# Optimization experiments

Measured on AMD Instinct MI355X. Metric: run time of the kernel, lower is better.

Reference implementation:

```python
import jax, jax.numpy as jnp
import numpy as np

D_MODEL, D_STATE, EXPAND = 1024, 64, 2
D_INNER = EXPAND * D_MODEL
BATCH, SEQ = 4, 2048


def setup_inputs() -> dict:
    key = jax.random.key(0)
    ks = jax.random.split(key, 7)
    s = lambda *d: 1.0 / np.sqrt(d[0])
    x = jax.random.normal(ks[0], (BATCH, SEQ, D_MODEL), dtype=jnp.float32)
    # weights stored as [in, out] so y = x @ W
    W_in = jax.random.normal(ks[1], (D_MODEL, 2 * D_INNER), dtype=jnp.float32) * s(D_MODEL)
    W_xp = jax.random.normal(ks[2], (D_INNER, 2 * D_STATE + 1), dtype=jnp.float32) * s(D_INNER)
    W_B = jax.random.normal(ks[3], (D_STATE, D_INNER), dtype=jnp.float32) * s(D_STATE)
    W_C = jax.random.normal(ks[4], (D_STATE, D_INNER), dtype=jnp.float32) * s(D_STATE)
    W_out = jax.random.normal(ks[5], (D_INNER, D_MODEL), dtype=jnp.float32) * s(D_INNER)
    D = jnp.ones((D_INNER,), dtype=jnp.float32)
    A_log = jnp.asarray(np.log(0.01), dtype=jnp.float32)
    return {"x": x, "W_in": W_in, "W_xp": W_xp, "W_B": W_B,
            "W_C": W_C, "W_out": W_out, "D": D, "A_log": A_log}


def _scan_recurrence(a, b):
    """h_t = a_t * h_{t-1} + b_t via associative scan over seq axis (axis=1).
    a, b: [B, S, D_inner]."""
    def combine(e1, e2):
        a1, b1 = e1
        a2, b2 = e2
        return a1 * a2, a2 * b1 + b2
    _, h = jax.lax.associative_scan(combine, (a, b), axis=1)
    return h


def reference(x, W_in, W_xp, W_B, W_C, W_out, D, A_log):
    xz = x @ W_in                               # [B,S,2*Di]
    xi, z = jnp.split(xz, 2, axis=-1)           # each [B,S,Di]
    proj = xi @ W_xp                            # [B,S,2*Ds+1]
    delta = jax.nn.softplus(proj[..., :1])      # [B,S,1]
    B_raw = proj[..., 1:1 + D_STATE]
    C_raw = proj[..., 1 + D_STATE:]
    B = B_raw @ W_B                             # [B,S,Di]
    C = C_raw @ W_C                             # [B,S,Di]
    A = -jnp.exp(A_log)                         # scalar
    A_bar = jnp.exp(delta * A)                  # [B,S,1]
    a = jnp.broadcast_to(A_bar, B.shape)        # [B,S,Di]
    h = _scan_recurrence(a, B * xi)             # [B,S,Di]
    y = C * h + D * xi                          # [B,S,Di]
    y = y * jax.nn.silu(z)
    return y @ W_out                            # [B,S,Dm]
```

## Files before the change

kernel.cpp:

```cpp
#include <hip/hip_runtime.h>
#include <hip/hip_bf16.h>
#include <cstdint>
#include <cstddef>

#define D_MODEL 1024
#define D_STATE 64
#define D_INNER 2048
#define BATCH   4
#define SEQ     2048
#define MROWS   (BATCH*SEQ)
#define CHUNK   32
#define NCHUNK  (SEQ/CHUNK)

typedef __bf16 bf16x8 __attribute__((ext_vector_type(8)));
typedef float  f32x4  __attribute__((ext_vector_type(4)));

__device__ __forceinline__ float bf2f(unsigned short u) {
    union { unsigned int i; float f; } v; v.i = ((unsigned int)u) << 16; return v.f;
}
__device__ __forceinline__ unsigned short f2bf(float f) {
    union { float f; unsigned int i; } v; v.f = f;
    unsigned int r = v.i + 0x7fff + ((v.i >> 16) & 1);
    return (unsigned short)(r >> 16);
}
__device__ __forceinline__ float lo16(unsigned u){ return bf2f((unsigned short)(u & 0xffffu)); }
__device__ __forceinline__ float hi16(unsigned u){ return bf2f((unsigned short)(u >> 16)); }
__device__ __forceinline__ unsigned pack2(float a, float b){
    return (unsigned)f2bf(a) | ((unsigned)f2bf(b) << 16);
}

__global__ __launch_bounds__(256) void f32_to_bf16(const float* __restrict__ in,
                                                   unsigned short* __restrict__ out) {
    size_t i = ((size_t)blockIdx.x * 256 + threadIdx.x) * 4;
    float4 v = *(const float4*)(in + i);
    uint2 o; o.x = pack2(v.x, v.y); o.y = pack2(v.z, v.w);
    *(uint2*)(out + i) = o;
}

__global__ void transpose_f32_bf16(const float* __restrict__ in,
                                   unsigned short* __restrict__ out, int rows, int cols) {
    __shared__ float t[32][33];
    int bx = blockIdx.x * 32, by = blockIdx.y * 32;
    int tx = threadIdx.x, ty = threadIdx.y;
    int r = by + ty, c = bx + tx;
    if (r < rows && c < cols) t[ty][tx] = in[(size_t)r * cols + c];
    __syncthreads();
    int ro = bx + ty, co = by + tx;
    if (ro < cols && co < rows) out[(size_t)ro * rows + co] = f2bf(t[tx][ty]);
}

__global__ void transpose_wxp(const float* __restrict__ wxp,
                              unsigned short* __restrict__ out) {
    __shared__ float t[32][33];
    int j0 = blockIdx.x * 32, k0 = blockIdx.y * 32;
    int tx = threadIdx.x, ty = threadIdx.y;
    t[ty][tx] = wxp[(size_t)(k0 + ty) * 129 + 1 + j0 + tx];
    __syncthreads();
    out[(size_t)(j0 + ty) * 2048 + k0 + tx] = f2bf(t[tx][ty]);
}

__global__ void extract_w0(const float* __restrict__ wxp, float* __restrict__ w0f) {
    int k = blockIdx.x * 256 + threadIdx.x;
    if (k < D_INNER) w0f[k] = wxp[(size_t)k * 129];
}

#define BM 128
#define BN 128
enum { EPI_PLAIN = 0, EPI_F32OUT = 3, EPI_F32ACC = 4 };

__device__ __forceinline__ void gload_lds16(const void* g, void* l) {
    __builtin_amdgcn_global_load_lds((const __attribute__((address_space(1))) void*)g,
                                     (__attribute__((address_space(3))) void*)l, 16, 0, 0);
}

template<int EPI>
__global__ __launch_bounds__(256) void gemm_tn(
    const unsigned short* __restrict__ A,
    const unsigned short* __restrict__ BT,
    void* __restrict__ Cv,
    int M, int N, int kchunk, int lda, int ldb, int ldc)
{
    __shared__ __align__(16) unsigned short As0[BM * 32];
    __shared__ __align__(16) unsigned short As1[BM * 32];
    __shared__ __align__(16) unsigned short Bs0[BN * 32];
    __shared__ __align__(16) unsigned short Bs1[BN * 32];
    const int tid  = threadIdx.x;
    const int wave = tid >> 6, lane = tid & 63;
    const int row0 = blockIdx.y * BM, col0 = blockIdx.x * BN;
    const int wr = (wave >> 1) * 64, wc = (wave & 1) * 64;
    const int srow = lane >> 2;
    const int scol = (lane & 3) * 8;

    f32x4 acc[4][4];
    #pragma unroll
    for (int i = 0; i < 4; ++i)
        #pragma unroll
        for (int j = 0; j < 4; ++j)
            #pragma unroll
            for (int r = 0; r < 4; ++r) acc[i][j][r] = 0.0f;

    const int kbeg = blockIdx.z * kchunk;
    for (int k0 = kbeg; k0 < kbeg + kchunk; k0 += 64) {
        #pragma unroll
        for (int qi = 0; qi < 2; ++qi) {
            int q = wave * 2 + qi;
            const unsigned short* gA = A  + (size_t)(row0 + q*16 + srow) * lda + (k0 + scol);
            const unsigned short* gB = BT + (size_t)(col0 + q*16 + srow) * ldb + (k0 + scol);
            gload_lds16(gA,      &As0[q * 512]);
            gload_lds16(gA + 32, &As1[q * 512]);
            gload_lds16(gB,      &Bs0[q * 512]);
            gload_lds16(gB + 32, &Bs1[q * 512]);
        }
        __syncthreads();
        bf16x8 af0[4], af1[4], bf0[4], bf1[4];
        const int lro = lane & 15, lko = (lane >> 4) * 8;
        #pragma unroll
        for (int t = 0; t < 4; ++t) {
            af0[t] = *(const bf16x8*)&As0[(wr + t*16 + lro) * 32 + lko];
            af1[t] = *(const bf16x8*)&As1[(wr + t*16 + lro) * 32 + lko];
            bf0[t] = *(const bf16x8*)&Bs0[(wc + t*16 + lro) * 32 + lko];
            bf1[t] = *(const bf16x8*)&Bs1[(wc + t*16 + lro) * 32 + lko];
        }
        #pragma unroll
        for (int i = 0; i < 4; ++i)
            #pragma unroll
            for (int j = 0; j < 4; ++j) {
                acc[i][j] = __builtin_amdgcn_mfma_f32_16x16x32_bf16(af0[i], bf0[j], acc[i][j], 0, 0, 0);
                acc[i][j] = __builtin_amdgcn_mfma_f32_16x16x32_bf16(af1[i], bf1[j], acc[i][j], 0, 0, 0);
            }
        __syncthreads();
    }

    const int r0 = (lane >> 4) * 4, cl = lane & 15;
    #pragma unroll
    for (int i = 0; i < 4; ++i) {
        #pragma unroll
        for (int j = 0; j < 4; ++j) {
            #pragma unroll
            for (int r = 0; r < 4; ++r) {
                int gr = row0 + wr + i*16 + r0 + r;
                int gc = col0 + wc + j*16 + cl;
                float v = acc[i][j][r];
                if (EPI == EPI_F32OUT)      ((float*)Cv)[(size_t)gr * ldc + gc] = v;
                else if (EPI == EPI_F32ACC) ((float*)Cv + (size_t)blockIdx.z * M * ldc)[(size_t)gr * ldc + gc] = v;
                else                        ((unsigned short*)Cv)[(size_t)gr * ldc + gc] = f2bf(v);
            }
        }
    }
}

__global__ __launch_bounds__(256) void reduce_proj(const float* __restrict__ part,
                                                   unsigned short* __restrict__ out) {
    size_t i = ((size_t)blockIdx.x * 256 + threadIdx.x) * 4;
    const size_t stride = (size_t)MROWS * 128;
    float4 s = *(const float4*)(part + i);
    #pragma unroll
    for (int p = 1; p < 4; ++p) {
        float4 v = *(const float4*)(part + p * stride + i);
        s.x += v.x; s.y += v.y; s.z += v.z; s.w += v.w;
    }
    uint2 o; o.x = pack2(s.x, s.y); o.y = pack2(s.z, s.w);
    *(uint2*)(out + i) = o;
}

__global__ __launch_bounds__(256) void delta_kernel(
    const unsigned short* __restrict__ xz, const float* __restrict__ w0f,
    const float* __restrict__ A_log,
    float* __restrict__ dA, float* __restrict__ abar)
{
    int row  = blockIdx.x * 4 + (threadIdx.x >> 6);
    int lane = threadIdx.x & 63;
    const unsigned short* xi = xz + (size_t)row * (2 * D_INNER);
    float s = 0.f;
    #pragma unroll
    for (int step = 0; step < 4; ++step) {
        int oct = step * 64 + lane;
        uint4 u = *(const uint4*)(xi + oct * 8);
        const float4* pw = (const float4*)(w0f + oct * 8);
        float4 wa = pw[0], wb = pw[1];
        s += lo16(u.x)*wa.x + hi16(u.x)*wa.y + lo16(u.y)*wa.z + hi16(u.y)*wa.w
           + lo16(u.z)*wb.x + hi16(u.z)*wb.y + lo16(u.w)*wb.z + hi16(u.w)*wb.w;
    }
    #pragma unroll
    for (int off = 32; off > 0; off >>= 1) s += __shfl_xor(s, off);
    if (lane == 0) {
        float Av = -expf(A_log[0]);
        float d  = (s > 20.f) ? s : log1pf(expf(s));
        float da = d * Av;
        dA[row] = da;
        abar[row] = expf(da);
    }
}

__global__ void chunk_aux(const float* __restrict__ dA,
                          float* __restrict__ sfx, float* __restrict__ P) {
    int idx = threadIdx.x;
    float suf = 0.f;
    for (int t = CHUNK - 1; t >= 0; --t) {
        sfx[idx * CHUNK + t] = expf(suf);
        suf += dA[idx * CHUNK + t];
    }
    P[idx] = expf(suf);
}

#define CB 128
#define R2 64
#define PST 136

__global__ __launch_bounds__(256) void bc_carry(
    const unsigned short* __restrict__ proj,
    const unsigned short* __restrict__ wbT,
    const unsigned short* __restrict__ xz,
    const float* __restrict__ sfx,
    float* __restrict__ carry)
{
    __shared__ unsigned short Ps[R2 * PST];
    __shared__ unsigned short Xs[R2 * PST];
    const int cb = blockIdx.x, j2 = blockIdx.y, b = blockIdx.z;
    const int c0 = cb * CB;
    const int srow = b * SEQ + j2 * R2;
    const int tid = threadIdx.x, wave = tid >> 6, lane = tid & 63;

    #pragma unroll
    for (int i = 0; i < 4; ++i) {
        int e = i * 2048 + tid * 8, r = e >> 7, c = e & 127;
        uint4 v = *(const uint4*)(proj + (size_t)(srow + r) * 128 + c);
        *(uint4*)&Ps[r * PST + c] = v;
    }
    #pragma unroll
    for (int i = 0; i < 4; ++i) {
        int e = i * 2048 + tid * 8, r = e >> 7, c = e & 127;
        uint4 v = *(const uint4*)(xz + (size_t)(srow + r) * (2*D_INNER) + c0 + c);
        *(uint4*)&Xs[r * PST + c] = v;
    }
    __syncthreads();

    const int mt0 = (wave >> 1) * 2;
    const int nb  = (wave & 1) * 64;
    const int lr = lane & 15, lq = lane >> 4;

    f32x4 acc[2][4];
    #pragma unroll
    for (int mi = 0; mi < 2; ++mi)
        #pragma unroll
        for (int ni = 0; ni < 4; ++ni)
            #pragma unroll
            for (int r = 0; r < 4; ++r) acc[mi][ni][r] = 0.0f;

    #pragma unroll
    for (int s = 0; s < 2; ++s) {
        bf16x8 af[2], bfr[4];
        #pragma unroll
        for (int mi = 0; mi < 2; ++mi)
            af[mi] = *(const bf16x8*)&Ps[((mt0+mi)*16 + lr) * PST + s*32 + lq*8];
        #pragma unroll
        for (int ni = 0; ni < 4; ++ni)
            bfr[ni] = *(const bf16x8*)(wbT + (size_t)(c0 + nb + ni*16 + lr) * 64 + s*32 + lq*8);
        #pragma unroll
        for (int mi = 0; mi < 2; ++mi)
            #pragma unroll
            for (int ni = 0; ni < 4; ++ni)
                acc[mi][ni] = __builtin_amdgcn_mfma_f32_16x16x32_bf16(af[mi], bfr[ni], acc[mi][ni], 0, 0, 0);
    }

    float w8[2][4];
    #pragma unroll
    for (int mi = 0; mi < 2; ++mi)
        #pragma unroll
        for (int r = 0; r < 4; ++r)
            w8[mi][r] = sfx[srow + (mt0+mi)*16 + lq*4 + r];

    float csum[4];
    #pragma unroll
    for (int ni = 0; ni < 4; ++ni) {
        float s = 0.f;
        #pragma unroll
        for (int mi = 0; mi < 2; ++mi)
            #pragma unroll
            for (int r = 0; r < 4; ++r) {
                int row = (mt0+mi)*16 + lq*4 + r;
                float xv = bf2f(Xs[row * PST + nb + ni*16 + lr]);
                s += w8[mi][r] * acc[mi][ni][r] * xv;
            }
        s += __shfl_xor(s, 16);
        s += __shfl_xor(s, 32);
        csum[ni] = s;
    }
    if (lane < 16) {
        int jj = j2 * 2 + (mt0 >> 1);
        float* dst = carry + ((size_t)(b * NCHUNK + jj)) * D_INNER + c0 + nb;
        #pragma unroll
        for (int ni = 0; ni < 4; ++ni) dst[ni*16 + lane] = csum[ni];
    }
}

__global__ __launch_bounds__(256) void scan_chunks(float* __restrict__ carry,
                                                   const float* __restrict__ P) {
    int c = blockIdx.x * 256 + threadIdx.x;
    int b = blockIdx.y;
    float H = 0.f;
    for (int j = 0; j < NCHUNK; ++j) {
        size_t idx = ((size_t)(b * NCHUNK + j)) * D_INNER + c;
        float cr = carry[idx];
        carry[idx] = H;
        H = P[b * NCHUNK + j] * H + cr;
    }
}

__global__ __launch_bounds__(256) void bc_scan(
    const unsigned short* __restrict__ proj,
    const unsigned short* __restrict__ wbT,
    const unsigned short* __restrict__ wcT,
    const unsigned short* __restrict__ xz,
    const float* __restrict__ Dvf,
    const float* __restrict__ abar,
    const float* __restrict__ carry,
    unsigned short* __restrict__ ypre)
{
    __shared__ unsigned short Ps[R2 * PST];
    __shared__ unsigned short Bt[R2 * PST];
    __shared__ unsigned short Ct[R2 * PST];
    const int cb = blockIdx.x, j2 = blockIdx.y, b = blockIdx.z;
    const int c0 = cb * CB;
    const int srow = b * SEQ + j2 * R2;
    const int tid = threadIdx.x, wave = tid >> 6, lane = tid & 63;

    #pragma unroll
    for (int i = 0; i < 4; ++i) {
        int e = i * 2048 + tid * 8, r = e >> 7, c = e & 127;
        uint4 v = *(const uint4*)(proj + (size_t)(srow + r) * 128 + c);
        *(uint4*)&Ps[r * PST + c] = v;
    }
    __syncthreads();

    const int mt0 = (wave >> 1) * 2;
    const int nb  = (wave & 1) * 64;
    const int lr = lane & 15, lq = lane >> 4;

    #pragma unroll
    for (int mat = 0; mat < 2; ++mat) {
        const unsigned short* W = mat ? wcT : wbT;
        unsigned short* dst = mat ? Ct : Bt;
        const int koff = mat ? 64 : 0;
        f32x4 acc[2][4];
        #pragma unroll
        for (int mi = 0; mi < 2; ++mi)
            #pragma unroll
            for (int ni = 0; ni < 4; ++ni)
                #pragma unroll
                for (int r = 0; r < 4; ++r) acc[mi][ni][r] = 0.0f;
        #pragma unroll
        for (int s = 0; s < 2; ++s) {
            bf16x8 af[2], bfr[4];
            #pragma unroll
            for (int mi = 0; mi < 2; ++mi)
                af[mi] = *(const bf16x8*)&Ps[((mt0+mi)*16 + lr) * PST + koff + s*32 + lq*8];
            #pragma unroll
            for (int ni = 0; ni < 4; ++ni)
                bfr[ni] = *(const bf16x8*)(W + (size_t)(c0 + nb + ni*16 + lr) * 64 + s*32 + lq*8);
            #pragma unroll
            for (int mi = 0; mi < 2; ++mi)
                #pragma unroll
                for (int ni = 0; ni < 4; ++ni)
                    acc[mi][ni] = __builtin_amdgcn_mfma_f32_16x16x32_bf16(af[mi], bfr[ni], acc[mi][ni], 0, 0, 0);
        }
        #pragma unroll
        for (int mi = 0; mi < 2; ++mi)
            #pragma unroll
            for (int ni = 0; ni < 4; ++ni)
                #pragma unroll
                for (int r = 0; r < 4; ++r) {
                    int row = (mt0+mi)*16 + lq*4 + r;
                    dst[row * PST + nb + ni*16 + lr] = f2bf(acc[mi][ni][r]);
                }
    }
    __syncthreads();

    const int c  = tid & 127;
    const int hh = tid >> 7;
    const int jj = j2 * 2 + hh;
    const int r0 = hh * 32;
    float h  = carry[((size_t)(b * NCHUNK + jj)) * D_INNER + c0 + c];
    float dv = Dvf[c0 + c];
    for (int t = 0; t < CHUNK; ++t) {
        int row = r0 + t;
        size_t m = (size_t)(srow + row);
        float a  = abar[m];
        float xv = bf2f(xz[m * (2*D_INNER) + c0 + c]);
        float zv = bf2f(xz[m * (2*D_INNER) + D_INNER + c0 + c]);
        float bv = bf2f(Bt[row * PST + c]);
        float cv = bf2f(Ct[row * PST + c]);
        h = fmaf(a, h, bv * xv);
        float y = cv * h + dv * xv;
        y *= zv / (1.f + expf(-zv));
        ypre[m * D_INNER + c0 + c] = f2bf(y);
    }
}

extern "C" void kernel_launch(void* const* d_in, const int* in_sizes, int n_in,
                              void* d_out, int out_size, void* d_ws, size_t ws_size,
                              hipStream_t stream) {
    const float* x     = (const float*)d_in[0];
    const float* W_in  = (const float*)d_in[1];
    const float* W_xp  = (const float*)d_in[2];
    const float* W_B   = (const float*)d_in[3];
    const float* W_C   = (const float*)d_in[4];
    const float* W_out = (const float*)d_in[5];
    const float* Dv    = (const float*)d_in[6];
    const float* A_log = (const float*)d_in[7];
    float* out = (float*)d_out;

    size_t off = 0;
    auto alloc = [&](size_t bytes) {
        void* p = (char*)d_ws + off; off += (bytes + 255) & ~(size_t)255; return p;
    };
    unsigned short* xbf   = (unsigned short*)alloc((size_t)MROWS * D_MODEL * 2);
    unsigned short* xz    = (unsigned short*)alloc((size_t)MROWS * 2 * D_INNER * 2);
    unsigned short* ypre  = (unsigned short*)alloc((size_t)MROWS * D_INNER * 2);
    unsigned short* winT  = (unsigned short*)alloc((size_t)4096 * 1024 * 2);
    unsigned short* woutT = (unsigned short*)alloc((size_t)1024 * 2048 * 2);
    unsigned short* wbT   = (unsigned short*)alloc((size_t)2048 * 64 * 2);
    unsigned short* wcT   = (unsigned short*)alloc((size_t)2048 * 64 * 2);
    unsigned short* wxpT  = (unsigned short*)alloc((size_t)128 * 2048 * 2);
    unsigned short* projb = (unsigned short*)alloc((size_t)MROWS * 128 * 2);
    float* proj_part = (float*)alloc((size_t)4 * MROWS * 128 * 4);
    float* w0f   = (float*)alloc(2048 * 4);
    float* dA    = (float*)alloc(MROWS * 4);
    float* abar  = (float*)alloc(MROWS * 4);
    float* sfx   = (float*)alloc(MROWS * 4);
    float* P     = (float*)alloc(BATCH * NCHUNK * 4);
    float* carry = (float*)alloc((size_t)BATCH * NCHUNK * D_INNER * 4);
    (void)ws_size; (void)n_in; (void)in_sizes; (void)out_size;

    hipLaunchKernelGGL(f32_to_bf16, dim3((MROWS * D_MODEL) / 1024), dim3(256), 0, stream, x, xbf);

    dim3 tb(32, 32);
    hipLaunchKernelGGL(transpose_f32_bf16, dim3(4096/32, 1024/32), tb, 0, stream, W_in,  winT, 1024, 4096);
    hipLaunchKernelGGL(transpose_f32_bf16, dim3(1024/32, 2048/32), tb, 0, stream, W_out, woutT, 2048, 1024);
    hipLaunchKernelGGL(transpose_f32_bf16, dim3(2048/32, 64/32),   tb, 0, stream, W_B,   wbT, 64, 2048);
    hipLaunchKernelGGL(transpose_f32_bf16, dim3(2048/32, 64/32),   tb, 0, stream, W_C,   wcT, 64, 2048);
    hipLaunchKernelGGL(transpose_wxp, dim3(4, 64), tb, 0, stream, W_xp, wxpT);
    hipLaunchKernelGGL(extract_w0, dim3(8), dim3(256), 0, stream, W_xp, w0f);

    hipLaunchKernelGGL((gemm_tn<EPI_PLAIN>), dim3(4096/BN, MROWS/BM), dim3(256), 0, stream,
                       xbf, winT, (void*)xz, MROWS, 4096, 1024, 1024, 1024, 4096);

    hipLaunchKernelGGL(delta_kernel, dim3(MROWS/4), dim3(256), 0, stream, xz, w0f, A_log, dA, abar);
    hipLaunchKernelGGL(chunk_aux, dim3(1), dim3(BATCH*NCHUNK), 0, stream, dA, sfx, P);

    hipLaunchKernelGGL((gemm_tn<EPI_F32ACC>), dim3(1, MROWS/BM, 4), dim3(256), 0, stream,
                       xz, wxpT, (void*)proj_part, MROWS, 128, 512, 2*D_INNER, D_INNER, 128);
    hipLaunchKernelGGL(reduce_proj, dim3((MROWS * 128) / 1024), dim3(256), 0, stream,
                       proj_part, projb);

    hipLaunchKernelGGL(bc_carry, dim3(D_INNER/CB, SEQ/R2, BATCH), dim3(256), 0, stream,
                       projb, wbT, xz, sfx, carry);
    hipLaunchKernelGGL(scan_chunks, dim3(D_INNER/256, BATCH), dim3(256), 0, stream, carry, P);
    hipLaunchKernelGGL(bc_scan, dim3(D_INNER/CB, SEQ/R2, BATCH), dim3(256), 0, stream,
                       projb, wbT, wcT, xz, Dv, abar, carry, ypre);

    hipLaunchKernelGGL((gemm_tn<EPI_F32OUT>), dim3(1024/BN, MROWS/BM), dim3(256), 0, stream,
                       ypre, woutT, (void*)out, MROWS, 1024, 2048, D_INNER, D_INNER, 1024);
}
```

Measured before the change: 357.6 us.

## Scan B/C directly from MFMA registers with shuffle-based chunk scan

The bc_scan kernel keeps the B and C projection accumulators in registers and no longer round-trips them through shared memory. Each lane runs the recurrence over its own 4 rows in the MFMA output layout. Cross-lane prefix combination uses __shfl_up, seeded with the chunk carry. The x slice and abar are staged in shared memory up front. The final D*x skip term, SiLU gate and store are done in a vectorized 8-wide pass. This is meant to cut the serial 32-step per-thread loop and its scattered global loads, at the cost of more register pressure and an extra bf16 rounding of C*h before the skip add.

```diff
diff --git a/kernel.cpp b/kernel.cpp
--- a/kernel.cpp
+++ b/kernel.cpp
@@ -318,8 +318,8 @@
     unsigned short* __restrict__ ypre)
 {
     __shared__ unsigned short Ps[R2 * PST];
-    __shared__ unsigned short Bt[R2 * PST];
-    __shared__ unsigned short Ct[R2 * PST];
+    __shared__ unsigned short Xs[R2 * PST];
+    __shared__ float Aab[R2];
     const int cb = blockIdx.x, j2 = blockIdx.y, b = blockIdx.z;
     const int c0 = cb * CB;
     const int srow = b * SEQ + j2 * R2;
@@ -331,69 +331,143 @@
         uint4 v = *(const uint4*)(proj + (size_t)(srow + r) * 128 + c);
         *(uint4*)&Ps[r * PST + c] = v;
     }
+    #pragma unroll
+    for (int i = 0; i < 4; ++i) {
+        int e = i * 2048 + tid * 8, r = e >> 7, c = e & 127;
+        uint4 v = *(const uint4*)(xz + (size_t)(srow + r) * (2*D_INNER) + c0 + c);
+        *(uint4*)&Xs[r * PST + c] = v;
+    }
+    if (tid < R2) Aab[tid] = abar[srow + tid];
     __syncthreads();
 
-    const int mt0 = (wave >> 1) * 2;
-    const int nb  = (wave & 1) * 64;
+    const int hh = wave >> 1;
+    const int nb = (wave & 1) * 64;
     const int lr = lane & 15, lq = lane >> 4;
-
-    #pragma unroll
-    for (int mat = 0; mat < 2; ++mat) {
-        const unsigned short* W = mat ? wcT : wbT;
-        unsigned short* dst = mat ? Ct : Bt;
-        const int koff = mat ? 64 : 0;
-        f32x4 acc[2][4];
+    const int jj = j2 * 2 + hh;
+
+    f32x4 accB[2][4], accC[2][4];
+    #pragma unroll
+    for (int mi = 0; mi < 2; ++mi)
+        #pragma unroll
+        for (int ni = 0; ni < 4; ++ni)
+            #pragma unroll
+            for (int r = 0; r < 4; ++r) { accB[mi][ni][r] = 0.f; accC[mi][ni][r] = 0.f; }
+    #pragma unroll
+    for (int s = 0; s < 2; ++s) {
+        bf16x8 afB[2], afC[2], bB[4], bC[4];
+        #pragma unroll
+        for (int mi = 0; mi < 2; ++mi) {
+            afB[mi] = *(const bf16x8*)&Ps[(hh*32 + mi*16 + lr) * PST + s*32 + lq*8];
+            afC[mi] = *(const bf16x8*)&Ps[(hh*32 + mi*16 + lr) * PST + 64 + s*32 + lq*8];
+        }
+        #pragma unroll
+        for (int ni = 0; ni < 4; ++ni) {
+            bB[ni] = *(const bf16x8*)(wbT + (size_t)(c0 + nb + ni*16 + lr) * 64 + s*32 + lq*8);
+            bC[ni] = *(const bf16x8*)(wcT + (size_t)(c0 + nb + ni*16 + lr) * 64 + s*32 + lq*8);
+        }
         #pragma unroll
         for (int mi = 0; mi < 2; ++mi)
             #pragma unroll
-            for (int ni = 0; ni < 4; ++ni)
-                #pragma unroll
-                for (int r = 0; r < 4; ++r) acc[mi][ni][r] = 0.0f;
-        #pragma unroll
-        for (int s = 0; s < 2; ++s) {
-            bf16x8 af[2], bfr[4];
-            #pragma unroll
-            for (int mi = 0; mi < 2; ++mi)
-                af[mi] = *(const bf16x8*)&Ps[((mt0+mi)*16 + lr) * PST + koff + s*32 + lq*8];
-            #pragma unroll
-            for (int ni = 0; ni < 4; ++ni)
-                bfr[ni] = *(const bf16x8*)(W + (size_t)(c0 + nb + ni*16 + lr) * 64 + s*32 + lq*8);
-            #pragma unroll
-            for (int mi = 0; mi < 2; ++mi)
-                #pragma unroll
-                for (int ni = 0; ni < 4; ++ni)
-                    acc[mi][ni] = __builtin_amdgcn_mfma_f32_16x16x32_bf16(af[mi], bfr[ni], acc[mi][ni], 0, 0, 0);
-        }
-        #pragma unroll
-        for (int mi = 0; mi < 2; ++mi)
-            #pragma unroll
-            for (int ni = 0; ni < 4; ++ni)
-                #pragma unroll
-                for (int r = 0; r < 4; ++r) {
-                    int row = (mt0+mi)*16 + lq*4 + r;
-                    dst[row * PST + nb + ni*16 + lr] = f2bf(acc[mi][ni][r]);
-                }
+            for (int ni = 0; ni < 4; ++ni) {
+                accB[mi][ni] = __builtin_amdgcn_mfma_f32_16x16x32_bf16(afB[mi], bB[ni], accB[mi][ni], 0, 0, 0);
+                accC[mi][ni] = __builtin_amdgcn_mfma_f32_16x16x32_bf16(afC[mi], bC[ni], accC[mi][ni], 0, 0, 0);
+            }
     }
     __syncthreads();
 
-    const int c  = tid & 127;
-    const int hh = tid >> 7;
-    const int jj = j2 * 2 + hh;
-    const int r0 = hh * 32;
-    float h  = carry[((size_t)(b * NCHUNK + jj)) * D_INNER + c0 + c];
-    float dv = Dvf[c0 + c];
-    for (int t = 0; t < CHUNK; ++t) {
-        int row = r0 + t;
-        size_t m = (size_t)(srow + row);
-        float a  = abar[m];
-        float xv = bf2f(xz[m * (2*D_INNER) + c0 + c]);
-        float zv = bf2f(xz[m * (2*D_INNER) + D_INNER + c0 + c]);
-        float bv = bf2f(Bt[row * PST + c]);
-        float cv = bf2f(Ct[row * PST + c]);
-        h = fmaf(a, h, bv * xv);
-        float y = cv * h + dv * xv;
-        y *= zv / (1.f + expf(-zv));
-        ypre[m * D_INNER + c0 + c] = f2bf(y);
+    float ar[2][4], pa[2][4];
+    #pragma unroll
+    for (int mi = 0; mi < 2; ++mi) {
+        float p = 1.f;
+        #pragma unroll
+        for (int r = 0; r < 4; ++r) {
+            ar[mi][r] = Aab[hh*32 + mi*16 + lq*4 + r];
+            p *= ar[mi][r];
+            pa[mi][r] = p;
+        }
+    }
+    float A0[2], A1[2], A2[2], exA[2];
+    #pragma unroll
+    for (int mi = 0; mi < 2; ++mi) {
+        A0[mi] = pa[mi][3];
+        float p = __shfl_up(A0[mi], 16);
+        A1[mi] = (lq >= 1) ? p * A0[mi] : A0[mi];
+        float p2 = __shfl_up(A1[mi], 32);
+        A2[mi] = (lq >= 2) ? p2 * A1[mi] : A1[mi];
+        float e = __shfl_up(A2[mi], 16);
+        exA[mi] = (lq == 0) ? 1.f : e;
+    }
+    const float TA = __shfl(A2[0], 48 + lr);
+
+    #pragma unroll
+    for (int ni = 0; ni < 4; ++ni) {
+        const int ch = nb + ni*16 + lr;
+        float H0 = carry[((size_t)(b * NCHUNK + jj)) * D_INNER + c0 + ch];
+        float hloc[2][4];
+        #pragma unroll
+        for (int mi = 0; mi < 2; ++mi) {
+            float h = 0.f;
+            #pragma unroll
+            for (int r = 0; r < 4; ++r) {
+                float xv = bf2f(Xs[(hh*32 + mi*16 + lq*4 + r) * PST + ch]);
+                h = fmaf(ar[mi][r], h, accB[mi][ni][r] * xv);
+                hloc[mi][r] = h;
+            }
+        }
+        float exB[2], TB = 0.f;
+        #pragma unroll
+        for (int mi = 0; mi < 2; ++mi) {
+            float Bv = hloc[mi][3];
+            float p = __shfl_up(Bv, 16);
+            if (lq >= 1) Bv = fmaf(A0[mi], p, Bv);
+            float p2 = __shfl_up(Bv, 32);
+            if (lq >= 2) Bv = fmaf(A1[mi], p2, Bv);
+            float e = __shfl_up(Bv, 16);
+            exB[mi] = (lq == 0) ? 0.f : e;
+            if (mi == 0) TB = __shfl(Bv, 48 + lr);
+        }
+        float hin0 = fmaf(exA[0], H0, exB[0]);
+        float Hmid = fmaf(TA, H0, TB);
+        float hin1 = fmaf(exA[1], Hmid, exB[1]);
+        #pragma unroll
+        for (int mi = 0; mi < 2; ++mi) {
+            float hin = mi ? hin1 : hin0;
+            #pragma unroll
+            for (int r = 0; r < 4; ++r) {
+                float h  = fmaf(pa[mi][r], hin, hloc[mi][r]);
+                float yc = accC[mi][ni][r] * h;
+                Ps[(hh*32 + mi*16 + lq*4 + r) * PST + ch] = f2bf(yc);
+            }
+        }
+    }
+    __syncthreads();
+
+    #pragma unroll
+    for (int p = 0; p < 4; ++p) {
+        int e = p * 2048 + tid * 8, r = e >> 7, c = e & 127;
+        uint4 yv = *(const uint4*)&Ps[r * PST + c];
+        uint4 xv = *(const uint4*)&Xs[r * PST + c];
+        float4 d0 = *(const float4*)(Dvf + c0 + c);
+        float4 d1 = *(const float4*)(Dvf + c0 + c + 4);
+        uint4 zv = *(const uint4*)(xz + (size_t)(srow + r) * (2*D_INNER) + D_INNER + c0 + c);
+        float y0 = lo16(yv.x) + d0.x * lo16(xv.x);
+        float y1 = hi16(yv.x) + d0.y * hi16(xv.x);
+        float y2 = lo16(yv.y) + d0.z * lo16(xv.y);
+        float y3 = hi16(yv.y) + d0.w * hi16(xv.y);
+        float y4 = lo16(yv.z) + d1.x * lo16(xv.z);
+        float y5 = hi16(yv.z) + d1.y * hi16(xv.z);
+        float y6 = lo16(yv.w) + d1.z * lo16(xv.w);
+        float y7 = hi16(yv.w) + d1.w * hi16(xv.w);
+        float z0 = lo16(zv.x), z1 = hi16(zv.x), z2 = lo16(zv.y), z3 = hi16(zv.y);
+        float z4 = lo16(zv.z), z5 = hi16(zv.z), z6 = lo16(zv.w), z7 = hi16(zv.w);
+        y0 *= z0 / (1.f + expf(-z0)); y1 *= z1 / (1.f + expf(-z1));
+        y2 *= z2 / (1.f + expf(-z2)); y3 *= z3 / (1.f + expf(-z3));
+        y4 *= z4 / (1.f + expf(-z4)); y5 *= z5 / (1.f + expf(-z5));
+        y6 *= z6 / (1.f + expf(-z6)); y7 *= z7 / (1.f + expf(-z7));
+        uint4 o;
+        o.x = pack2(y0, y1); o.y = pack2(y2, y3);
+        o.z = pack2(y4, y5); o.w = pack2(y6, y7);
+        *(uint4*)(ypre + (size_t)(srow + r) * D_INNER + c0 + c) = o;
     }
 }
 
```

Result: no change. 358.3 us (+0.2%).
